# Optimization experiments

Hardware: AMD Instinct MI355X
Metric: run time of the kernel (lower is better)

## Reference

```python
import jax, jax.numpy as jnp
import numpy as np

H = 16          # n_heads
DH = 128        # head_dim
DR = 64         # rope_dim
DC = DH - DR    # content_dim = 64
THETA = 10000.0
SCALE = 1.0 / np.sqrt(DH)


def _rope_tables(T, dtype):
    inv = 1.0 / (THETA ** (jnp.arange(0, DR, 2, dtype=jnp.float32) / DR))  # [DR/2]
    t = jnp.arange(T, dtype=jnp.float32)
    freqs = jnp.outer(t, inv)  # [T, DR/2]
    return jnp.cos(freqs).astype(dtype), jnp.sin(freqs).astype(dtype)


def _apply_rope(x, cos, sin):
    # x: [B,H,T,DR]; cos/sin: [T,DR/2] broadcast over B,H
    d = x.shape[-1] // 2
    x1, x2 = x[..., :d], x[..., d:]
    return jnp.concatenate([x1 * cos - x2 * sin, x1 * sin + x2 * cos], axis=-1)


def setup_inputs() -> dict:
    key = jax.random.key(0)
    ks = jax.random.split(key, 9)
    B, T, D = 1, 2048, 2048
    s = 0.02
    return {
        "x": jax.random.normal(ks[0], (B, T, D), jnp.float32),
        "Wq_down": jax.random.normal(ks[1], (D, 512), jnp.float32) * s,
        "Wq_up": jax.random.normal(ks[2], (512, H * DC), jnp.float32) * s,
        "Wq_rope": jax.random.normal(ks[3], (D, H * DR), jnp.float32) * s,
        "Wkv_down": jax.random.normal(ks[4], (D, 512), jnp.float32) * s,
        "Wk_up": jax.random.normal(ks[5], (512, H * DC), jnp.float32) * s,
        "Wv_up": jax.random.normal(ks[6], (512, H * DH), jnp.float32) * s,
        "Wk_rope": jax.random.normal(ks[7], (D, H * DR), jnp.float32) * s,
        "Wo": jax.random.normal(ks[8], (H * DH, D), jnp.float32) * s,
    }


def reference(x, Wq_down, Wq_up, Wq_rope, Wkv_down, Wk_up, Wv_up, Wk_rope, Wo):
    B, T, D = x.shape
    # low-rank query path: down then up, content part only
    q_content = ((x @ Wq_down) @ Wq_up).reshape(B, T, H, DC).transpose(0, 2, 1, 3)
    q_pos = (x @ Wq_rope).reshape(B, T, H, DR).transpose(0, 2, 1, 3)
    kv_latent = x @ Wkv_down                    # [B,T,d_latent]
    k_pos = (x @ Wk_rope).reshape(B, T, H, DR).transpose(0, 2, 1, 3)

    cos, sin = _rope_tables(T, x.dtype)
    q_pos = _apply_rope(q_pos, cos, sin)
    k_pos = _apply_rope(k_pos, cos, sin)

    k_content = (kv_latent @ Wk_up).reshape(B, T, H, DC).transpose(0, 2, 1, 3)
    v = (kv_latent @ Wv_up).reshape(B, T, H, DH).transpose(0, 2, 1, 3)

    q = jnp.concatenate([q_content, q_pos], axis=-1)  # [B,H,T,DH]
    k = jnp.concatenate([k_content, k_pos], axis=-1)  # [B,H,T,DH]

    scores = jnp.einsum("bhtd,bhsd->bhts", q, k) * SCALE
    causal = jnp.tril(jnp.ones((T, T), dtype=bool))
    scores = jnp.where(causal, scores, jnp.finfo(scores.dtype).min)
    attn = jax.nn.softmax(scores, axis=-1)
    out = jnp.einsum("bhts,bhsd->bhtd", attn, v)       # [B,H,T,DH]
    out = out.transpose(0, 2, 1, 3).reshape(B, T, H * DH)
    return out @ Wo
```

## Files before the change

kernel.cpp:

```cpp
#include <hip/hip_runtime.h>
#include <math.h>

#define T_SEQ 2048
#define D_MODEL 2048
#define H_HEADS 16
#define DH 128
#define DR 64
#define DC 64
#define D_LAT 512
#define SEGLEN 7
#define NSEG_TOT 46
#define NSEG_OF(q) ((2 * (q) + 2 + SEGLEN - 1) / SEGLEN)
#define QSCALE (0.08838834764831845f * 1.4426950408889634f)

typedef __attribute__((ext_vector_type(8))) short short8;
typedef __attribute__((ext_vector_type(4))) short short4v;
typedef __attribute__((ext_vector_type(4))) float f32x4;

#if __has_builtin(__builtin_amdgcn_exp2f)
#define EXP2(x) __builtin_amdgcn_exp2f(x)
#else
#define EXP2(x) exp2f(x)
#endif

__device__ __forceinline__ float bf2f(short b) {
    unsigned u = ((unsigned)(unsigned short)b) << 16;
    return __builtin_bit_cast(float, u);
}
__device__ __forceinline__ short f2bf(float f) {
    unsigned u = __builtin_bit_cast(unsigned, f);
    unsigned r = u + 0x7fffu + ((u >> 16) & 1u);
    return (short)(r >> 16);
}
__device__ __forceinline__ short f2bf_trunc(float f) {
    return (short)(__builtin_bit_cast(unsigned, f) >> 16);
}

#define GLD_LDS(gp, lp) \
    __builtin_amdgcn_global_load_lds( \
        (const __attribute__((address_space(1))) void*)(gp), \
        (__attribute__((address_space(3))) void*)(lp), 16, 0, 0)

__device__ __forceinline__ void ct_tile(float (*tile)[33],
                                        const float* __restrict__ W,
                                        short* __restrict__ Wt,
                                        int R, int C, int ldo, int rel) {
    int bx = rel % (C / 32), by = rel / (C / 32);
    int c0 = bx * 32, r0 = by * 32;
    int tx = threadIdx.x & 31, ty = threadIdx.x >> 5;
    #pragma unroll
    for (int i = 0; i < 4; ++i)
        tile[ty + i * 8][tx] = W[(size_t)(r0 + ty + i * 8) * C + c0 + tx];
    __syncthreads();
    #pragma unroll
    for (int i = 0; i < 4; ++i)
        Wt[(size_t)(c0 + ty + i * 8) * ldo + r0 + tx] = f2bf(tile[tx][ty + i * 8]);
    __syncthreads();
}

__global__ __launch_bounds__(256) void prep(const float* __restrict__ x,
                                            short* __restrict__ xb,
                                            const float* __restrict__ Wqd,
                                            const float* __restrict__ Wkvd,
                                            const float* __restrict__ Wqr,
                                            const float* __restrict__ Wkr,
                                            const float* __restrict__ Wqu,
                                            const float* __restrict__ Wku,
                                            const float* __restrict__ Wvu,
                                            const float* __restrict__ Wo,
                                            short* __restrict__ WdT,
                                            short* __restrict__ WupT2,
                                            short* __restrict__ WoT) {
    __shared__ float tile[32][33];
    int bid = blockIdx.x;
    if (bid < 4096) {
        int i = bid * 1024 + threadIdx.x * 4;
        float4 f = *(const float4*)&x[i];
        short4v o;
        o.x = f2bf(f.x); o.y = f2bf(f.y); o.z = f2bf(f.z); o.w = f2bf(f.w);
        *(short4v*)&xb[i] = o;
    } else if (bid < 5120) {
        ct_tile(tile, Wqd,  WdT + (size_t)0 * 2048,    2048, 512,  2048, bid - 4096);
    } else if (bid < 6144) {
        ct_tile(tile, Wkvd, WdT + (size_t)512 * 2048,  2048, 512,  2048, bid - 5120);
    } else if (bid < 8192) {
        ct_tile(tile, Wqr,  WdT + (size_t)1024 * 2048, 2048, 1024, 2048, bid - 6144);
    } else if (bid < 10240) {
        ct_tile(tile, Wkr,  WdT + (size_t)2048 * 2048, 2048, 1024, 2048, bid - 8192);
    } else if (bid < 10752) {
        ct_tile(tile, Wqu,  WupT2 + (size_t)0 * 512,    512, 1024, 512, bid - 10240);
    } else if (bid < 11264) {
        ct_tile(tile, Wku,  WupT2 + (size_t)1024 * 512, 512, 1024, 512, bid - 10752);
    } else if (bid < 12288) {
        ct_tile(tile, Wvu,  WupT2 + (size_t)2048 * 512, 512, 2048, 512, bid - 11264);
    } else {
        ct_tile(tile, Wo,   WoT, 2048, 2048, 2048, bid - 12288);
    }
}

__global__ __launch_bounds__(256) void transpose_bf16(const short* __restrict__ in,
                                                      short* __restrict__ outb,
                                                      int ldi) {
    __shared__ short tile[64][65];
    int c0 = blockIdx.x * 64, t0 = blockIdx.y * 64;
    int tx = threadIdx.x & 31, ty = threadIdx.x >> 5;
    #pragma unroll
    for (int i = 0; i < 8; ++i) {
        int r = ty + i * 8;
        int vv = *(const int*)&in[(size_t)(t0 + r) * ldi + c0 + tx * 2];
        tile[r][tx * 2]     = (short)(vv & 0xffff);
        tile[r][tx * 2 + 1] = (short)(((unsigned)vv) >> 16);
    }
    __syncthreads();
    #pragma unroll
    for (int i = 0; i < 8; ++i) {
        int c = ty + i * 8;
        unsigned lo = (unsigned short)tile[tx * 2][c];
        unsigned hi = (unsigned short)tile[tx * 2 + 1][c];
        *(int*)&outb[(size_t)(c0 + c) * 2048 + t0 + tx * 2] = (int)(lo | (hi << 16));
    }
}

__global__ __launch_bounds__(256) void gemm_bt(const short* __restrict__ A,
                                               const short* __restrict__ A2,
                                               const short* __restrict__ Bt,
                                               short* __restrict__ C0,
                                               short* __restrict__ C1,
                                               short* __restrict__ C2,
                                               short* __restrict__ C3,
                                               int N, int Kblk,
                                               int lda, int ldb, int ldc,
                                               int ncut, int scut, float cscale) {
    __shared__ short As[128 * 32];
    __shared__ short Bs[128 * 32];
    const int tid = threadIdx.x;
    const int wave = tid >> 6, lane = tid & 63;
    const int lin = blockIdx.x;
    const int X = N >> 7, Xq = X >> 2;
    const int xcd = lin & 7;
    int r = lin >> 3;
    const int bx = (xcd & 3) * Xq + (r % Xq); r /= Xq;
    const int by = (xcd >> 2) * 8 + (r & 7);
    const int bz = r >> 3;
    const int row0 = by * 128, col0 = bx * 128;
    const int kbase = bz * Kblk;
    const short* Ause = (col0 < ncut) ? A : A2;
    short* Cuse = (bz == 0) ? C0 : (bz == 1) ? C1 : (bz == 2) ? C2 : C3;
    const int wr = (wave >> 1) * 64, wc = (wave & 1) * 64;
    const int lr = lane & 15, quad = lane >> 4;

    f32x4 acc[4][4];
    #pragma unroll
    for (int i = 0; i < 4; ++i)
        #pragma unroll
        for (int j = 0; j < 4; ++j) acc[i][j] = (f32x4){0.f, 0.f, 0.f, 0.f};

    for (int k0 = kbase; k0 < kbase + Kblk; k0 += 32) {
        __syncthreads();
        #pragma unroll
        for (int it = 0; it < 2; ++it) {
            int idx = wave * 64 + it * 256 + lane;
            const short* ga = Ause + (size_t)(row0 + (idx >> 2)) * lda + k0 + (idx & 3) * 8;
            const short* gb = Bt   + (size_t)(col0 + (idx >> 2)) * ldb + k0 + (idx & 3) * 8;
            int lds0 = (wave * 64 + it * 256) * 8;
            GLD_LDS(ga, &As[lds0]);
            GLD_LDS(gb, &Bs[lds0]);
        }
        __syncthreads();

        short8 af[4], bfr[4];
        #pragma unroll
        for (int i = 0; i < 4; ++i)
            af[i] = *(const short8*)&As[(wr + i * 16 + lr) * 32 + quad * 8];
        #pragma unroll
        for (int j = 0; j < 4; ++j)
            bfr[j] = *(const short8*)&Bs[(wc + j * 16 + lr) * 32 + quad * 8];
        #pragma unroll
        for (int i = 0; i < 4; ++i)
            #pragma unroll
            for (int j = 0; j < 4; ++j)
                acc[i][j] = __builtin_amdgcn_mfma_f32_16x16x32_bf16(af[i], bfr[j],
                                                                   acc[i][j], 0, 0, 0);
    }

    const float sc = (col0 < scut) ? cscale : 1.0f;
    #pragma unroll
    for (int i = 0; i < 4; ++i) {
        int rb = row0 + wr + i * 16 + quad * 4;
        #pragma unroll
        for (int j = 0; j < 4; ++j) {
            int c = col0 + wc + j * 16 + lr;
            #pragma unroll
            for (int rr = 0; rr < 4; ++rr)
                Cuse[(size_t)(rb + rr) * ldc + c] = f2bf(acc[i][j][rr] * sc);
        }
    }
}

__global__ __launch_bounds__(192) void finish_down(short* __restrict__ cat,
                                                   const short* __restrict__ pdown) {
    const int t = blockIdx.x;
    const int k8 = threadIdx.x * 8;
    const int c0 = ((k8 >> 5) << 6) + (k8 & 31);
    const size_t lo = (size_t)t * 3072 + c0;
    const size_t hi = lo + 32;
    short8 al = *(const short8*)&cat[lo];
    short8 ah = *(const short8*)&cat[hi];
    short8 bl = *(const short8*)&pdown[lo];
    short8 bh = *(const short8*)&pdown[hi];
    float xl[8], xh[8];
    #pragma unroll
    for (int j = 0; j < 8; ++j) {
        xl[j] = bf2f(al[j]) + bf2f(bl[j]);
        xh[j] = bf2f(ah[j]) + bf2f(bh[j]);
    }
    if (c0 >= 1024) {
        float sc = (c0 < 2048) ? QSCALE : 1.0f;
        #pragma unroll
        for (int j = 0; j < 8; ++j) {
            int i = (c0 & 31) + j;
            float freq = (float)t * __powf(10000.0f, -(float)i / 32.0f);
            float cs = __cosf(freq), sn = __sinf(freq);
            float r1 = (xl[j] * cs - xh[j] * sn) * sc;
            float r2 = (xl[j] * sn + xh[j] * cs) * sc;
            xl[j] = r1; xh[j] = r2;
        }
    }
    short8 ol, oh;
    #pragma unroll
    for (int j = 0; j < 8; ++j) { ol[j] = f2bf(xl[j]); oh[j] = f2bf(xh[j]); }
    *(short8*)&cat[lo] = ol;
    *(short8*)&cat[hi] = oh;
}

__global__ __launch_bounds__(256) void add_out_f32(const short* __restrict__ p0,
                                                   const short* __restrict__ p1,
                                                   float* __restrict__ out) {
    int i = (blockIdx.x * 256 + threadIdx.x) * 4;
    short4v a = *(const short4v*)&p0[i];
    short4v b = *(const short4v*)&p1[i];
    float4 o;
    o.x = bf2f(a.x) + bf2f(b.x);
    o.y = bf2f(a.y) + bf2f(b.y);
    o.z = bf2f(a.z) + bf2f(b.z);
    o.w = bf2f(a.w) + bf2f(b.w);
    *(float4*)&out[i] = o;
}

__global__ __launch_bounds__(256) void attn_mla_split(const short* __restrict__ qkup,
                                                      const short* __restrict__ cat,
                                                      const short* __restrict__ vT,
                                                      short* __restrict__ slabA,
                                                      short* __restrict__ slabB,
                                                      float* __restrict__ lpart) {
    const int lin = blockIdx.x;
    const int xcd = lin & 7;
    int k_ = lin >> 3;
    const int h = xcd + 8 * (k_ & 1);
    const int pp = k_ >> 1;
    int qt = 0, s = 0, acc = 0;
    #pragma unroll
    for (int q = 0; q < 16; ++q) {
        const int ns = NSEG_OF(q);
        if (pp >= acc) { qt = q; s = pp - acc; }
        acc += ns;
    }
    const int nchunk = 2 * qt + 2;
    const int nsq = NSEG_OF(qt);
    const int cbase = nchunk / nsq, crem = nchunk % nsq;
    const int c0 = s * cbase + (s < crem ? s : crem);
    const int c1 = c0 + cbase + (s < crem ? 1 : 0);

    const int tid = threadIdx.x;
    const int wave = tid >> 6, lane = tid & 63;
    const int lr = lane & 15, quad = lane >> 4;

    __shared__ short Ks[2][32 * 128];
    __shared__ short Vst[2][128 * 32];
    __shared__ short Ps[4][2][16 * 40];

    const short8 ones = {0x3F80, 0x3F80, 0x3F80, 0x3F80,
                         0x3F80, 0x3F80, 0x3F80, 0x3F80};

    const int Q0 = qt * 128;
    const int qrowA = Q0 + wave * 16;
    const int qrowB = qrowA + 64;

    short8 qf[2][4];
    #pragma unroll
    for (int sb = 0; sb < 2; ++sb) {
        int t = (sb ? qrowB : qrowA) + lr;
        #pragma unroll
        for (int kci = 0; kci < 4; ++kci) {
            const short* src = (kci < 2)
                ? qkup + (size_t)t * 4096 + h * 64
                : cat + (size_t)t * 3072 + 1024 + h * 64;
            qf[sb][kci] = *(const short8*)&src[(kci & 1) * 32 + quad * 8];
        }
    }

    const int idx = wave * 64 + lane;
    const int key = idx >> 4;
    const int cg = (idx & 15) ^ (key & 15);
    const short* kp0 = (cg < 8)
        ? qkup + (size_t)key * 4096 + 1024 + h * 64 + cg * 8
        : cat + (size_t)key * 3072 + 2048 + h * 64 + (cg - 8) * 8;
    const int kst = (cg < 8) ? 4096 : 3072;
    const short* kp1 = kp0 + (size_t)16 * kst;
    const int dd = idx >> 2;
    const int scg = (idx & 3) ^ (dd & 3);
    const short* vp0 = vT + (size_t)(h * 128 + dd) * 2048 + scg * 8;
    const short* vp1 = vp0 + (size_t)64 * 2048;
    kp0 += (size_t)c0 * 64 * kst; kp1 += (size_t)c0 * 64 * kst;
    vp0 += c0 * 64;               vp1 += c0 * 64;
    const int kadv = 64 * kst;
    const int vadv = 64;
    const int kph = 32 * kst;
    const int ldsA = (wave * 64) * 8;
    const int ldsB = (wave * 64 + 256) * 8;

    f32x4 Oacc[2][8];
    #pragma unroll
    for (int sb = 0; sb < 2; ++sb)
        #pragma unroll
        for (int d = 0; d < 8; ++d) Oacc[sb][d] = (f32x4){0.f, 0.f, 0.f, 0.f};
    f32x4 Lacc[2];
    Lacc[0] = (f32x4){0.f, 0.f, 0.f, 0.f};
    Lacc[1] = (f32x4){0.f, 0.f, 0.f, 0.f};

    for (int cc = c0; cc < c1; ++cc) {
        __syncthreads();
        GLD_LDS(kp0,       &Ks[0][ldsA]);
        GLD_LDS(kp1,       &Ks[0][ldsB]);
        GLD_LDS(kp0 + kph, &Ks[1][ldsA]);
        GLD_LDS(kp1 + kph, &Ks[1][ldsB]);
        GLD_LDS(vp0,       &Vst[0][ldsA]);
        GLD_LDS(vp1,       &Vst[0][ldsB]);
        GLD_LDS(vp0 + 32,  &Vst[1][ldsA]);
        GLD_LDS(vp1 + 32,  &Vst[1][ldsB]);
        kp0 += kadv; kp1 += kadv; vp0 += vadv; vp1 += vadv;
        __syncthreads();

        #pragma unroll
        for (int half = 0; half < 2; ++half) {
            const int s0 = cc * 64 + half * 32;
            if (s0 > qrowB + 15) continue;
            const bool actA = (s0 <= qrowA + 15);
            const short* Kc = Ks[half];
            const short* Vc = Vst[half];

            f32x4 sacc[2][2];
            #pragma unroll
            for (int sb = 0; sb < 2; ++sb)
                #pragma unroll
                for (int n = 0; n < 2; ++n) sacc[sb][n] = (f32x4){0.f, 0.f, 0.f, 0.f};
            #pragma unroll
            for (int n = 0; n < 2; ++n) {
                #pragma unroll
                for (int kci = 0; kci < 4; ++kci) {
                    short8 kf = *(const short8*)
                        &Kc[(n * 16 + lr) * 128 + ((kci * 4 + quad) ^ lr) * 8];
                    if (actA)
                        sacc[0][n] = __builtin_amdgcn_mfma_f32_16x16x32_bf16(
                            qf[0][kci], kf, sacc[0][n], 0, 0, 0);
                    sacc[1][n] = __builtin_amdgcn_mfma_f32_16x16x32_bf16(
                        qf[1][kci], kf, sacc[1][n], 0, 0, 0);
                }
            }
            #pragma unroll
            for (int sb = 0; sb < 2; ++sb) {
                if (sb == 0 && !actA) continue;
                const int qrow0 = sb ? qrowB : qrowA;
                if (s0 + 31 > qrow0) {
                    #pragma unroll
                    for (int r = 0; r < 4; ++r) {
                        int qg = qrow0 + quad * 4 + r;
                        #pragma unroll
                        for (int n = 0; n < 2; ++n) {
                            int sidx = s0 + n * 16 + lr;
                            sacc[sb][n][r] = (sidx <= qg) ? sacc[sb][n][r] : -1e30f;
                        }
                    }
                }
                #pragma unroll
                for (int r = 0; r < 4; ++r) {
                    Ps[wave][sb][(quad * 4 + r) * 40 + lr] =
                        f2bf_trunc(EXP2(sacc[sb][0][r]));
                    Ps[wave][sb][(quad * 4 + r) * 40 + 16 + lr] =
                        f2bf_trunc(EXP2(sacc[sb][1][r]));
                }
            }
            short8 pfA, pfB;
            if (actA) {
                pfA = *(const short8*)&Ps[wave][0][lr * 40 + quad * 8];
                Lacc[0] = __builtin_amdgcn_mfma_f32_16x16x32_bf16(pfA, ones,
                                                                  Lacc[0], 0, 0, 0);
            }
            pfB = *(const short8*)&Ps[wave][1][lr * 40 + quad * 8];
            Lacc[1] = __builtin_amdgcn_mfma_f32_16x16x32_bf16(pfB, ones,
                                                              Lacc[1], 0, 0, 0);
            #pragma unroll
            for (int dt = 0; dt < 8; ++dt) {
                short8 vf = *(const short8*)
                    &Vc[(dt * 16 + lr) * 32 + (quad ^ (lr & 3)) * 8];
                if (actA)
                    Oacc[0][dt] = __builtin_amdgcn_mfma_f32_16x16x32_bf16(
                        pfA, vf, Oacc[0][dt], 0, 0, 0);
                Oacc[1][dt] = __builtin_amdgcn_mfma_f32_16x16x32_bf16(
                    pfB, vf, Oacc[1][dt], 0, 0, 0);
            }
        }
    }

    const int slot = h * NSEG_TOT + pp;
    short* slotp = (slot < 512) ? slabA + (size_t)slot * 16384
                                : slabB + (size_t)(slot - 512) * 16384;
    #pragma unroll
    for (int sb = 0; sb < 2; ++sb) {
        const int rbase = wave * 16 + sb * 64 + quad * 4;
        #pragma unroll
        for (int r = 0; r < 4; ++r) {
            #pragma unroll
            for (int dt = 0; dt < 8; ++dt)
                slotp[(rbase + r) * 128 + dt * 16 + lr] = f2bf(Oacc[sb][dt][r]);
        }
        if (lr == 0) {
            #pragma unroll
            for (int r = 0; r < 4; ++r)
                lpart[(size_t)slot * 128 + rbase + r] = Lacc[sb][r];
        }
    }
}

__global__ __launch_bounds__(256) void attn_combine(const short* __restrict__ slabA,
                                                    const short* __restrict__ slabB,
                                                    const float* __restrict__ lpart,
                                                    short* __restrict__ ao) {
    const int t = blockIdx.x;
    const int qt = t >> 7, rl = t & 127;
    const int h = threadIdx.x >> 4;
    const int di = (threadIdx.x & 15) * 8;
    int pf = 0;
    #pragma unroll
    for (int q = 0; q < 16; ++q)
        if (q < qt) pf += NSEG_OF(q);
    const int ns = NSEG_OF(qt);
    float o[8] = {0.f, 0.f, 0.f, 0.f, 0.f, 0.f, 0.f, 0.f};
    float den = 0.f;
    for (int s = 0; s < ns; ++s) {
        const int slot = h * NSEG_TOT + pf + s;
        const short* sp = (slot < 512) ? slabA + (size_t)slot * 16384
                                       : slabB + (size_t)(slot - 512) * 16384;
        short8 v = *(const short8*)&sp[rl * 128 + di];
        #pragma unroll
        for (int j = 0; j < 8; ++j) o[j] += bf2f(v[j]);
        den += lpart[(size_t)slot * 128 + rl];
    }
    float inv = 1.0f / den;
    short8 ov;
    #pragma unroll
    for (int j = 0; j < 8; ++j) ov[j] = f2bf(o[j] * inv);
    *(short8*)&ao[(size_t)t * 2048 + h * 128 + di] = ov;
}

extern "C" void kernel_launch(void* const* d_in, const int* in_sizes, int n_in,
                              void* d_out, int out_size, void* d_ws, size_t ws_size,
                              hipStream_t stream) {
    const float* x        = (const float*)d_in[0];
    const float* Wq_down  = (const float*)d_in[1];
    const float* Wq_up    = (const float*)d_in[2];
    const float* Wq_rope  = (const float*)d_in[3];
    const float* Wkv_down = (const float*)d_in[4];
    const float* Wk_up    = (const float*)d_in[5];
    const float* Wv_up    = (const float*)d_in[6];
    const float* Wk_rope  = (const float*)d_in[7];
    const float* Wo       = (const float*)d_in[8];
    float* out = (float*)d_out;

    short* p = (short*)d_ws;
    short* xb     = p; p += (size_t)2048 * 2048;
    short* WoT    = p; p += (size_t)2048 * 2048;
    short* cat    = p; p += (size_t)2048 * 3072;
    short* upcat2 = p; p += (size_t)2048 * 4096;
    short* WdT    = p; p += (size_t)3072 * 2048;
    short* WupT2  = p; p += (size_t)4096 * 512;
    short* vT     = p; p += (size_t)2048 * 2048;
    float* lpart  = (float*)p;
    short* pdown   = upcat2;
    short* aob     = cat;
    short* slabA   = WdT;
    short* slabB   = xb;
    short* pw0     = upcat2;
    short* pw1     = upcat2 + (size_t)2048 * 2048;

    prep<<<dim3(16384), 256, 0, stream>>>(x, xb, Wq_down, Wkv_down, Wq_rope,
                                          Wk_rope, Wq_up, Wk_up, Wv_up, Wo,
                                          WdT, WupT2, WoT);

    gemm_bt<<<dim3(24 * 16 * 2), 256, 0, stream>>>(xb, xb, WdT, cat, pdown,
                                                   nullptr, nullptr,
                                                   3072, 1024,
                                                   2048, 2048, 3072, 1 << 30, 0, 1.f);

    finish_down<<<dim3(2048), 192, 0, stream>>>(cat, pdown);

    gemm_bt<<<dim3(32 * 16 * 1), 256, 0, stream>>>(cat, cat + 512, WupT2,
                                                   upcat2, nullptr, nullptr, nullptr,
                                                   4096, 512,
                                                   3072, 512, 4096, 1024, 1024, QSCALE);

    transpose_bf16<<<dim3(32, 32), 256, 0, stream>>>(upcat2 + 2048, vT, 4096);

    attn_mla_split<<<dim3(16 * NSEG_TOT), 256, 0, stream>>>(upcat2, cat, vT,
                                                            slabA, slabB, lpart);
    attn_combine<<<dim3(2048), 256, 0, stream>>>(slabA, slabB, lpart, aob);

    gemm_bt<<<dim3(16 * 16 * 2), 256, 0, stream>>>(aob, aob, WoT, pw0, pw1,
                                                   nullptr, nullptr,
                                                   2048, 1024,
                                                   2048, 2048, 2048, 1 << 30, 0, 1.f);
    add_out_f32<<<dim3(2048 * 2048 / 1024), 256, 0, stream>>>(pw0, pw1, out);
}
```

Before: 274.4 us.

## Store V transposed in chunked pre-swizzled layout and pack P stores

The V transpose kernel now writes V in a per-head, per-32-key-chunk layout that is already swizzled, so each attention chunk's V tile is one contiguous region. The attention kernel can then fetch it with a single base pointer and fixed offsets instead of strided row loads. Separately, the bf16 softmax probabilities are packed two per 32-bit LDS store instead of two 16-bit stores. This targets global-load efficiency and LDS store count, at the cost of more complex index math in the transpose, and it relies on the packed P layout matching what the later reads expect.

```diff
diff --git a/kernel.cpp b/kernel.cpp
--- a/kernel.cpp
+++ b/kernel.cpp
@@ -32,8 +32,8 @@
     unsigned r = u + 0x7fffu + ((u >> 16) & 1u);
     return (short)(r >> 16);
 }
-__device__ __forceinline__ short f2bf_trunc(float f) {
-    return (short)(__builtin_bit_cast(unsigned, f) >> 16);
+__device__ __forceinline__ unsigned f2bf_tru(float f) {
+    return __builtin_bit_cast(unsigned, f) >> 16;
 }
 
 #define GLD_LDS(gp, lp) \
@@ -99,7 +99,7 @@
 }
 
 __global__ __launch_bounds__(256) void transpose_bf16(const short* __restrict__ in,
-                                                      short* __restrict__ outb,
+                                                      short* __restrict__ vTc,
                                                       int ldi) {
     __shared__ short tile[64][65];
     int c0 = blockIdx.x * 64, t0 = blockIdx.y * 64;
@@ -114,10 +114,19 @@
     __syncthreads();
     #pragma unroll
     for (int i = 0; i < 8; ++i) {
-        int c = ty + i * 8;
-        unsigned lo = (unsigned short)tile[tx * 2][c];
-        unsigned hi = (unsigned short)tile[tx * 2 + 1][c];
-        *(int*)&outb[(size_t)(c0 + c) * 2048 + t0 + tx * 2] = (int)(lo | (hi << 16));
+        int G = i * 256 + threadIdx.x;
+        int ch2 = G >> 10;
+        int rem = G & 1023;
+        int dl = rem >> 4;
+        int mp = rem & 15;
+        int dval = c0 + dl;
+        int h = dval >> 7, d128 = dval & 127;
+        int kl = 4 * ((mp >> 2) ^ (d128 & 3)) + (mp & 3);
+        unsigned lo = (unsigned short)tile[ch2 * 32 + kl][dl];
+        unsigned hi = (unsigned short)tile[ch2 * 32 + kl + 16][dl];
+        int chg = (t0 >> 5) + ch2;
+        size_t off = ((size_t)(h * 64 + chg)) * 4096 + d128 * 32 + mp * 2;
+        *(int*)&vTc[off] = (int)(lo | (hi << 16));
     }
 }
 
@@ -249,7 +258,7 @@
 
 __global__ __launch_bounds__(256) void attn_mla_split(const short* __restrict__ qkup,
                                                       const short* __restrict__ cat,
-                                                      const short* __restrict__ vT,
+                                                      const short* __restrict__ vTc,
                                                       short* __restrict__ slabA,
                                                       short* __restrict__ slabB,
                                                       float* __restrict__ lpart) {
@@ -307,14 +316,9 @@
         : cat + (size_t)key * 3072 + 2048 + h * 64 + (cg - 8) * 8;
     const int kst = (cg < 8) ? 4096 : 3072;
     const short* kp1 = kp0 + (size_t)16 * kst;
-    const int dd = idx >> 2;
-    const int scg = (idx & 3) ^ (dd & 3);
-    const short* vp0 = vT + (size_t)(h * 128 + dd) * 2048 + scg * 8;
-    const short* vp1 = vp0 + (size_t)64 * 2048;
+    const short* vp0 = vTc + ((size_t)h * 64 + (size_t)c0 * 2) * 4096 + idx * 8;
     kp0 += (size_t)c0 * 64 * kst; kp1 += (size_t)c0 * 64 * kst;
-    vp0 += c0 * 64;               vp1 += c0 * 64;
     const int kadv = 64 * kst;
-    const int vadv = 64;
     const int kph = 32 * kst;
     const int ldsA = (wave * 64) * 8;
     const int ldsB = (wave * 64 + 256) * 8;
@@ -330,15 +334,15 @@
 
     for (int cc = c0; cc < c1; ++cc) {
         __syncthreads();
-        GLD_LDS(kp0,       &Ks[0][ldsA]);
-        GLD_LDS(kp1,       &Ks[0][ldsB]);
-        GLD_LDS(kp0 + kph, &Ks[1][ldsA]);
-        GLD_LDS(kp1 + kph, &Ks[1][ldsB]);
-        GLD_LDS(vp0,       &Vst[0][ldsA]);
-        GLD_LDS(vp1,       &Vst[0][ldsB]);
-        GLD_LDS(vp0 + 32,  &Vst[1][ldsA]);
-        GLD_LDS(vp1 + 32,  &Vst[1][ldsB]);
-        kp0 += kadv; kp1 += kadv; vp0 += vadv; vp1 += vadv;
+        GLD_LDS(kp0,        &Ks[0][ldsA]);
+        GLD_LDS(kp1,        &Ks[0][ldsB]);
+        GLD_LDS(kp0 + kph,  &Ks[1][ldsA]);
+        GLD_LDS(kp1 + kph,  &Ks[1][ldsB]);
+        GLD_LDS(vp0,        &Vst[0][ldsA]);
+        GLD_LDS(vp0 + 2048, &Vst[0][ldsB]);
+        GLD_LDS(vp0 + 4096, &Vst[1][ldsA]);
+        GLD_LDS(vp0 + 6144, &Vst[1][ldsB]);
+        kp0 += kadv; kp1 += kadv; vp0 += 8192;
         __syncthreads();
 
         #pragma unroll
@@ -384,10 +388,9 @@
                 }
                 #pragma unroll
                 for (int r = 0; r < 4; ++r) {
-                    Ps[wave][sb][(quad * 4 + r) * 40 + lr] =
-                        f2bf_trunc(EXP2(sacc[sb][0][r]));
-                    Ps[wave][sb][(quad * 4 + r) * 40 + 16 + lr] =
-                        f2bf_trunc(EXP2(sacc[sb][1][r]));
+                    unsigned pk = f2bf_tru(EXP2(sacc[sb][0][r])) |
+                                  (f2bf_tru(EXP2(sacc[sb][1][r])) << 16);
+                    *(unsigned*)&Ps[wave][sb][(quad * 4 + r) * 40 + lr * 2] = pk;
                 }
             }
             short8 pfA, pfB;
@@ -484,7 +487,7 @@
     short* upcat2 = p; p += (size_t)2048 * 4096;
     short* WdT    = p; p += (size_t)3072 * 2048;
     short* WupT2  = p; p += (size_t)4096 * 512;
-    short* vT     = p; p += (size_t)2048 * 2048;
+    short* vTc    = p; p += (size_t)2048 * 2048;
     float* lpart  = (float*)p;
     short* pdown   = upcat2;
     short* aob     = cat;
@@ -509,9 +512,9 @@
                                                    4096, 512,
                                                    3072, 512, 4096, 1024, 1024, QSCALE);
 
-    transpose_bf16<<<dim3(32, 32), 256, 0, stream>>>(upcat2 + 2048, vT, 4096);
-
-    attn_mla_split<<<dim3(16 * NSEG_TOT), 256, 0, stream>>>(upcat2, cat, vT,
+    transpose_bf16<<<dim3(32, 32), 256, 0, stream>>>(upcat2 + 2048, vTc, 4096);
+
+    attn_mla_split<<<dim3(16 * NSEG_TOT), 256, 0, stream>>>(upcat2, cat, vTc,
                                                             slabA, slabB, lpart);
     attn_combine<<<dim3(2048), 256, 0, stream>>>(slabA, slabB, lpart, aob);
 
```

After: 272.1 us. Within noise of the previous version (-0.9%).
